# Kernel tuning notes

Hardware: AMD Instinct MI355X
Metric: run time of the kernel (lower is better)

## Reference

```python
import jax, jax.numpy as jnp
import numpy as np

N_E = 1024     # codebook size (n_e, nbooks=1)
E_DIM = 256    # embedding dim
BETA = 0.25
B, T = 16, 4096


def setup_inputs() -> dict:
    key = jax.random.key(0)
    k1, k2 = jax.random.split(key)
    z = jax.random.normal(k1, (B, T, E_DIM), dtype=jnp.float32)
    # matches torch init: uniform(-1/n_e_i, 1/n_e_i)
    codebook = jax.random.uniform(k2, (N_E, E_DIM), dtype=jnp.float32,
                                  minval=-1.0 / N_E, maxval=1.0 / N_E)
    return {"z": z, "codebook": codebook}


def reference(z, codebook):
    zf = z.reshape(-1, E_DIM)                                   # [N, d]
    dist = (jnp.sum(zf * zf, axis=1, keepdims=True)
            - 2.0 * (zf @ codebook.T)
            + jnp.sum(codebook * codebook, axis=1)[None, :])
    idx = jnp.argmin(dist, axis=1)                              # [N]
    # one-hot scatter + matmul == codebook gather
    z_q = codebook[idx].reshape(z.shape)                        # [B, T, d]
    loss = (jnp.mean((z_q - jax.lax.stop_gradient(z)) ** 2)
            + BETA * jnp.mean((z - jax.lax.stop_gradient(z_q)) ** 2))
    # straight-through estimator
    z_q_st = z + jax.lax.stop_gradient(z_q - z)
    indices = idx.reshape(z.shape[:-1] + (1,))                  # [B, T, 1]
    return z_q_st, loss, indices
```

## Files before the change

kernel.cpp:

```cpp
#include <hip/hip_runtime.h>
#include <hip/hip_bf16.h>
#include <math.h>

typedef __bf16 bf16x8 __attribute__((ext_vector_type(8)));
typedef float f32x4 __attribute__((ext_vector_type(4)));
typedef unsigned short u16x8 __attribute__((ext_vector_type(8)));

constexpr int EDIM = 256;
constexpr int NE = 1024;
constexpr int NROWS = 65536;
constexpr float BETA = 0.25f;

constexpr size_t A2T_OFF   = 0;
constexpr size_t A2T_SZ    = (size_t)1024 * 16 * 4096;
constexpr size_t B2T_OFF   = A2T_OFF + A2T_SZ;
constexpr size_t B2T_SZ    = (size_t)8 * 16 * 8192;
constexpr size_t SZROW_OFF = B2T_OFF + B2T_SZ;
constexpr size_t SZABS_OFF = SZROW_OFF + 262144;
constexpr size_t CNORM_OFF = SZABS_OFF + 262144;
constexpr size_t BMAX_OFF  = CNORM_OFF + 4096;
constexpr size_t EMAX_OFF  = BMAX_OFF + 4096;
constexpr size_t CNT_OFF   = EMAX_OFF + 256;
constexpr size_t LIST_OFF  = CNT_OFF + 256;
constexpr size_t LPART_OFF = LIST_OFF + 262144;
constexpr size_t LP2_OFF   = LPART_OFF + 262144;
constexpr size_t WS_NEED   = LP2_OFF + 1024;

__device__ __forceinline__ unsigned short f32_to_bf16_rne(float f) {
    unsigned u = __float_as_uint(f);
    u += 0x7fffu + ((u >> 16) & 1u);
    return (unsigned short)(u >> 16);
}
__device__ __forceinline__ float bf16_to_f32(unsigned short h) {
    return __uint_as_float((unsigned)h << 16);
}

#define GLL16(g, l)                                                                   \
    __builtin_amdgcn_global_load_lds(                                                 \
        (const __attribute__((address_space(1))) unsigned int*)(g),                   \
        (__attribute__((address_space(3))) unsigned int*)(l), 16, 0, 0)

__global__ __launch_bounds__(64)
void p3_codebook(const float* __restrict__ cb, float* __restrict__ cnorm,
                 char* __restrict__ B2t, float* __restrict__ bmax) {
    __shared__ float xr[256];
    __shared__ float rres[16];
    __shared__ unsigned short ehi[256], elo[256];
    const int e = blockIdx.x, l = threadIdx.x;
    const float4 v = reinterpret_cast<const float4*>(cb + (size_t)e * EDIM)[l];
    *reinterpret_cast<float4*>(&xr[l * 4]) = v;
    float amax = fmaxf(fmaxf(fabsf(v.x), fabsf(v.y)), fmaxf(fabsf(v.z), fabsf(v.w)));
    #pragma unroll
    for (int off = 32; off; off >>= 1) amax = fmaxf(amax, __shfl_down(amax, off));
    __syncthreads();
    #pragma unroll
    for (int i = 0; i < 4; ++i) {
        const int idx = i * 64 + l;
        const float f = xr[idx];
        const unsigned short h = f32_to_bf16_rne(f);
        ehi[idx] = h;
        elo[idx] = f32_to_bf16_rne(f - bf16_to_f32(h));
    }
    if (l < 16) {
        const float* x = xr + (l >> 3) * 128;
        const int j = l & 7;
        float r = __fmul_rn(x[j], x[j]);
        for (int i = 8; i < 128; i += 8) r = __fadd_rn(r, __fmul_rn(x[i + j], x[i + j]));
        rres[l] = r;
    }
    __syncthreads();
    if (l == 0) {
        float h0 = __fadd_rn(__fadd_rn(__fadd_rn(rres[0], rres[1]), __fadd_rn(rres[2], rres[3])),
                             __fadd_rn(__fadd_rn(rres[4], rres[5]), __fadd_rn(rres[6], rres[7])));
        float h1 = __fadd_rn(__fadd_rn(__fadd_rn(rres[8], rres[9]), __fadd_rn(rres[10], rres[11])),
                             __fadd_rn(__fadd_rn(rres[12], rres[13]), __fadd_rn(rres[14], rres[15])));
        cnorm[e] = __fadd_rn(h0, h1);
        bmax[e] = amax;
    }
    {
        const int c = l >> 2, kgv = l & 3;
        const int colbase = ((c < 8) ? c * 32 : (c - 8) * 32) + kgv * 8;
        const unsigned short* src = (c < 8) ? ehi : elo;
        char* dst = B2t + ((((size_t)(e >> 7) * 16 + c) * 512 + (size_t)kgv * 128 + (e & 127)) * 16);
        *reinterpret_cast<uint4*>(dst) = *reinterpret_cast<const uint4*>(&src[colbase]);
    }
}

__global__ void k_emax(const float* __restrict__ bmax, float* __restrict__ emax, int* cnt) {
    __shared__ float red[256];
    if (threadIdx.x == 0) cnt[0] = 0;
    float m = 0.f;
    for (int i = threadIdx.x; i < NE; i += 256) m = fmaxf(m, bmax[i]);
    red[threadIdx.x] = m;
    __syncthreads();
    for (int h = 128; h; h >>= 1) {
        if (threadIdx.x < h) red[threadIdx.x] = fmaxf(red[threadIdx.x], red[threadIdx.x + h]);
        __syncthreads();
    }
    if (threadIdx.x == 0) emax[0] = red[0];
}

__global__ __launch_bounds__(256)
void p2_atile(const float* __restrict__ z, char* __restrict__ A2t,
              float* __restrict__ szrow, float* __restrict__ szabs) {
    __shared__ float t[64][260];
    __shared__ float ch[64][16];
    const int mt = blockIdx.x, h = blockIdx.y, tid = threadIdx.x;
    const int mt64 = mt * 2 + h;
    const int row0 = mt64 * 64;
    #pragma unroll
    for (int i = 0; i < 16; ++i) {
        const int fid = i * 256 + tid;
        const int r = fid >> 6, c4 = fid & 63;
        const float4 v = *reinterpret_cast<const float4*>(
            z + (size_t)(row0 + r) * EDIM + c4 * 4);
        *reinterpret_cast<float4*>(&t[r][c4 * 4]) = v;
    }
    __syncthreads();
    {
        const int r = tid >> 2, q = tid & 3;
        float asum = 0.f;
        for (int c = 0; c < 64; ++c) asum += fabsf(t[r][q * 64 + c]);
        asum += __shfl_xor(asum, 1);
        asum += __shfl_xor(asum, 2);
        #pragma unroll
        for (int cc = 0; cc < 4; ++cc) {
            const int chain = q * 4 + cc;
            const float* x = &t[r][(chain >> 3) * 128];
            const int j = chain & 7;
            float rr = __fmul_rn(x[j], x[j]);
            for (int i = 8; i < 128; i += 8) rr = __fadd_rn(rr, __fmul_rn(x[i + j], x[i + j]));
            ch[r][chain] = rr;
        }
        __syncthreads();
        if (q == 0) {
            const float* c0 = ch[r];
            const float h0 = __fadd_rn(__fadd_rn(__fadd_rn(c0[0], c0[1]), __fadd_rn(c0[2], c0[3])),
                                       __fadd_rn(__fadd_rn(c0[4], c0[5]), __fadd_rn(c0[6], c0[7])));
            const float h1 = __fadd_rn(__fadd_rn(__fadd_rn(c0[8], c0[9]), __fadd_rn(c0[10], c0[11])),
                                       __fadd_rn(__fadd_rn(c0[12], c0[13]), __fadd_rn(c0[14], c0[15])));
            szrow[row0 + r] = __fadd_rn(h0, h1);
            szabs[row0 + r] = asum;
        }
    }
    #pragma unroll
    for (int i = 0; i < 16; ++i) {
        const int sid = i * 256 + tid;
        const int ca = sid >> 8, kgv = (sid >> 6) & 3, rwl = sid & 63;
        const int cbase = ((ca < 8) ? ca : ca - 8) * 32 + kgv * 8;
        u16x8 out;
        #pragma unroll
        for (int j = 0; j < 8; ++j) {
            const float f = t[rwl][cbase + j];
            unsigned short h16 = f32_to_bf16_rne(f);
            if (ca >= 8) h16 = f32_to_bf16_rne(f - bf16_to_f32(h16));
            out[j] = h16;
        }
        char* dst = A2t + ((((size_t)mt64 * 16 + ca) * 256 + (size_t)kgv * 64 + rwl) * 16);
        *reinterpret_cast<u16x8*>(dst) = out;
    }
}

__global__ __launch_bounds__(256, 2)
void vq_main(const char* __restrict__ A2t, const char* __restrict__ B2t,
             const float* __restrict__ cnorm, const float* __restrict__ szrow,
             const float* __restrict__ szabs, const float* __restrict__ emaxp,
             const float* __restrict__ cb,
             float* __restrict__ idxf, int* __restrict__ cnt, int* __restrict__ list,
             float* __restrict__ zq, float* __restrict__ lpart) {
    constexpr int CNS = 65536;
    __shared__ char smem[69632] __attribute__((aligned(16)));
    float* cns = reinterpret_cast<float*>(smem + CNS);
    float (*ms1)[2] = reinterpret_cast<float(*)[2]>(smem);
    float (*ms2)[2] = reinterpret_cast<float(*)[2]>(smem + 512);
    int   (*mi1)[2] = reinterpret_cast<int(*)[2]>(smem + 1024);
    int*  bidx      = reinterpret_cast<int*>(smem + 1536);

    const int tid = threadIdx.x;
    const int mtile = blockIdx.x;
    const size_t rowbase = (size_t)mtile * 64;
    const int l = tid & 63, wid = tid >> 6;
    const int kg = l >> 4, li = l & 15;
    const int wr = wid >> 1, wc = wid & 1;

    GLL16((const char*)cnorm + tid * 16, smem + CNS + tid * 16);
    const char* Ag = A2t + (size_t)mtile * 65536;
    #pragma unroll
    for (int i = 0; i < 16; ++i)
        GLL16(Ag + (i * 256 + tid) * 16, smem + (i * 256 + tid) * 16);
    asm volatile("s_waitcnt vmcnt(0)" ::: "memory");
    __syncthreads();

    int aoff[2], boff[4];
    #pragma unroll
    for (int f = 0; f < 2; ++f)
        aoff[f] = kg * 1024 + (wr * 32 + f * 16 + li) * 16;
    #pragma unroll
    for (int f = 0; f < 4; ++f)
        boff[f] = kg * 2048 + (wc * 64 + f * 16 + li) * 16;

    bf16x8 cAh[2], cAl[2], cB[4];
    #pragma unroll
    for (int f = 0; f < 2; ++f) {
        cAh[f] = *reinterpret_cast<const bf16x8*>(smem + 0 * 4096 + aoff[f]);
        cAl[f] = *reinterpret_cast<const bf16x8*>(smem + 8 * 4096 + aoff[f]);
    }
    #pragma unroll
    for (int f = 0; f < 4; ++f)
        cB[f] = *reinterpret_cast<const bf16x8*>(B2t + boff[f]);

    float s1v[2][4], s2v[2][4];
    int i1v[2][4];
    #pragma unroll
    for (int a = 0; a < 2; ++a)
        #pragma unroll
        for (int b = 0; b < 4; ++b) { s1v[a][b] = 3.4e38f; s2v[a][b] = 3.4e38f; i1v[a][b] = 0; }

    for (int nt = 0; nt < 8; ++nt) {
        f32x4 acc[2][4];
        const f32x4 zf4 = {0.f, 0.f, 0.f, 0.f};
        #pragma unroll
        for (int a = 0; a < 2; ++a)
            #pragma unroll
            for (int b = 0; b < 4; ++b) acc[a][b] = zf4;

        #pragma unroll
        for (int j = 0; j < 16; ++j) {
            const int g = nt * 16 + j;
            bf16x8 nAh[2], nAl[2], nB[4];
            {
                const int jn = (j + 1) & 15;
                const char* gB = B2t + (size_t)(g + 1) * 8192;
                #pragma unroll
                for (int f = 0; f < 4; ++f)
                    nB[f] = *reinterpret_cast<const bf16x8*>(gB + boff[f]);
                if (jn < 8) {
                    #pragma unroll
                    for (int f = 0; f < 2; ++f) {
                        nAh[f] = *reinterpret_cast<const bf16x8*>(smem + jn * 4096 + aoff[f]);
                        nAl[f] = *reinterpret_cast<const bf16x8*>(smem + (8 + jn) * 4096 + aoff[f]);
                    }
                } else {
                    #pragma unroll
                    for (int f = 0; f < 2; ++f) {
                        nAh[f] = *reinterpret_cast<const bf16x8*>(smem + (jn - 8) * 4096 + aoff[f]);
                        nAl[f] = cAl[f];
                    }
                }
            }
            #pragma unroll
            for (int fm = 0; fm < 2; ++fm)
                #pragma unroll
                for (int fn = 0; fn < 4; ++fn)
                    acc[fm][fn] = __builtin_amdgcn_mfma_f32_16x16x32_bf16(cAh[fm], cB[fn], acc[fm][fn], 0, 0, 0);
            if (j < 8) {
                #pragma unroll
                for (int fm = 0; fm < 2; ++fm)
                    #pragma unroll
                    for (int fn = 0; fn < 4; ++fn)
                        acc[fm][fn] = __builtin_amdgcn_mfma_f32_16x16x32_bf16(cAl[fm], cB[fn], acc[fm][fn], 0, 0, 0);
            }
            #pragma unroll
            for (int f = 0; f < 2; ++f) { cAh[f] = nAh[f]; cAl[f] = nAl[f]; }
            #pragma unroll
            for (int f = 0; f < 4; ++f) cB[f] = nB[f];
        }

        const int ntb = nt * 128;
        #pragma unroll
        for (int fn = 0; fn < 4; ++fn) {
            const int e = ntb + wc * 64 + fn * 16 + li;
            const float cn = cns[e];
            #pragma unroll
            for (int fm = 0; fm < 2; ++fm)
                #pragma unroll
                for (int r = 0; r < 4; ++r) {
                    const float s = cn - 2.0f * acc[fm][fn][r];
                    if (s < s1v[fm][r]) { s2v[fm][r] = s1v[fm][r]; s1v[fm][r] = s; i1v[fm][r] = e; }
                    else s2v[fm][r] = fminf(s2v[fm][r], s);
                }
        }
    }

    __syncthreads();

    #pragma unroll
    for (int fm = 0; fm < 2; ++fm)
        #pragma unroll
        for (int r = 0; r < 4; ++r) {
            float s1 = s1v[fm][r], s2 = s2v[fm][r];
            int i1 = i1v[fm][r];
            #pragma unroll
            for (int off = 1; off < 16; off <<= 1) {
                const float os1 = __shfl_xor(s1, off);
                const float os2 = __shfl_xor(s2, off);
                const int oi1 = __shfl_xor(i1, off);
                const bool take = (os1 < s1) || (os1 == s1 && oi1 < i1);
                const float loser = take ? s1 : os1;
                if (take) { s1 = os1; i1 = oi1; }
                s2 = fminf(fminf(s2, os2), loser);
            }
            if (li == 0) {
                const int rloc = wr * 32 + fm * 16 + (kg << 2) + r;
                ms1[rloc][wc] = s1; ms2[rloc][wc] = s2; mi1[rloc][wc] = i1;
            }
        }
    __syncthreads();

    if (tid < 64) {
        const float a1 = ms1[tid][0], b1 = ms1[tid][1];
        const float a2 = ms2[tid][0], b2 = ms2[tid][1];
        const int ai = mi1[tid][0], bi = mi1[tid][1];
        const bool take = (b1 < a1) || (b1 == a1 && bi < ai);
        const float s1 = take ? b1 : a1;
        const int i1 = take ? bi : ai;
        const float loser = take ? a1 : b1;
        const float s2 = fminf(fminf(a2, b2), loser);
        const int rowg = (int)rowbase + tid;
        const float szv = szrow[rowg], sab = szabs[rowg];
        const float M = 2.0e-4f * sab * emaxp[0] + ldexpf(1.0f, ilogbf(szv * 1.02f) - 23);
        idxf[rowg] = (float)i1;
        lpart[rowg] = s1 + szv;
        bidx[tid] = i1;
        if (s2 - s1 <= 2.0f * M) { const int p = atomicAdd(cnt, 1); list[p] = rowg; }
    }
    __syncthreads();

    {
        const float4* cb4 = reinterpret_cast<const float4*>(cb);
        float4* zq4 = reinterpret_cast<float4*>(zq);
        #pragma unroll 4
        for (int j = 0; j < 16; ++j) {
            const int rr = wid * 16 + j;
            const int e = bidx[rr];
            zq4[(rowbase + rr) * 64 + l] = cb4[(size_t)e * 64 + l];
        }
    }
}

__global__ __launch_bounds__(256)
void vq_rescan(const float* __restrict__ z, const float* __restrict__ cb,
               const float* __restrict__ cnorm, const float* __restrict__ szrow,
               const int* __restrict__ list, const int* __restrict__ cntp,
               float* __restrict__ idxf, float* __restrict__ zq, float* __restrict__ lpart) {
    __shared__ float zr[8][260];
    __shared__ float szs[8];
    __shared__ int rows_s[8];
    __shared__ float sred[256];
    __shared__ int ired[256];
    const int tid = threadIdx.x;
    const int n = cntp[0];
    const int groups = (n + 7) >> 3;
    for (int g = blockIdx.x; g < groups; g += gridDim.x) {
        if (tid < 8) {
            const int gi = g * 8 + tid;
            const int row = (gi < n) ? list[gi] : -1;
            rows_s[tid] = row;
            szs[tid] = (row >= 0) ? szrow[row] : 0.f;
        }
        __syncthreads();
        #pragma unroll
        for (int i = 0; i < 8; ++i) {
            const int sid = i * 256 + tid;
            const int rr = sid >> 8, k = sid & 255;
            if (rows_s[rr] >= 0) zr[rr][k] = z[(size_t)rows_s[rr] * EDIM + k];
        }
        __syncthreads();
        float bs[8];
        int bi[8];
        #pragma unroll
        for (int rr = 0; rr < 8; ++rr) { bs[rr] = 3.4e38f; bi[rr] = 0; }
        for (int q = 0; q < 4; ++q) {
            const int e = tid + q * 256;
            const float4* crow = reinterpret_cast<const float4*>(cb + (size_t)e * EDIM);
            float d[8];
            #pragma unroll
            for (int rr = 0; rr < 8; ++rr) d[rr] = 0.f;
            for (int k4 = 0; k4 < 64; ++k4) {
                const float4 c4 = crow[k4];
                #pragma unroll
                for (int rr = 0; rr < 8; ++rr) {
                    d[rr] = fmaf(zr[rr][k4 * 4 + 0], c4.x, d[rr]);
                    d[rr] = fmaf(zr[rr][k4 * 4 + 1], c4.y, d[rr]);
                    d[rr] = fmaf(zr[rr][k4 * 4 + 2], c4.z, d[rr]);
                    d[rr] = fmaf(zr[rr][k4 * 4 + 3], c4.w, d[rr]);
                }
            }
            const float cn = cnorm[e];
            #pragma unroll
            for (int rr = 0; rr < 8; ++rr) {
                const float b1 = __fadd_rn(szs[rr], __fmul_rn(-2.0f, d[rr]));
                const float s = __fadd_rn(b1, cn);
                if (s < bs[rr]) { bs[rr] = s; bi[rr] = e; }
            }
        }
        #pragma unroll
        for (int rr = 0; rr < 8; ++rr) {
            sred[tid] = bs[rr];
            ired[tid] = bi[rr];
            __syncthreads();
            for (int h = 128; h; h >>= 1) {
                if (tid < h) {
                    const float so = sred[tid + h];
                    const int io = ired[tid + h];
                    if (so < sred[tid] || (so == sred[tid] && io < ired[tid])) {
                        sred[tid] = so; ired[tid] = io;
                    }
                }
                __syncthreads();
            }
            if (rows_s[rr] >= 0) {
                const int best = ired[0];
                const int row = rows_s[rr];
                zq[(size_t)row * EDIM + tid] = cb[(size_t)best * EDIM + tid];
                if (tid == 0) { idxf[row] = (float)best; lpart[row] = sred[0]; }
            }
            __syncthreads();
        }
    }
}

__global__ void vq_loss1(const float* __restrict__ lpart, float* __restrict__ lp2) {
    __shared__ float red[256];
    const int t = threadIdx.x;
    red[t] = lpart[blockIdx.x * 256 + t];
    __syncthreads();
    for (int h = 128; h; h >>= 1) {
        if (t < h) red[t] += red[t + h];
        __syncthreads();
    }
    if (t == 0) lp2[blockIdx.x] = red[0];
}
__global__ void vq_loss2(const float* __restrict__ lp2, float* __restrict__ outloss) {
    __shared__ float red[256];
    const int t = threadIdx.x;
    red[t] = lp2[t];
    __syncthreads();
    for (int h = 128; h; h >>= 1) {
        if (t < h) red[t] += red[t + h];
        __syncthreads();
    }
    if (t == 0) outloss[0] = red[0] * ((1.0f + BETA) / 16777216.0f);
}

__device__ __forceinline__ float np_sum128_sq(const float* __restrict__ x) {
    float r[8];
    #pragma unroll
    for (int j = 0; j < 8; ++j) r[j] = __fmul_rn(x[j], x[j]);
    #pragma unroll
    for (int i = 8; i < 128; i += 8)
        #pragma unroll
        for (int j = 0; j < 8; ++j) r[j] = __fadd_rn(r[j], __fmul_rn(x[i + j], x[i + j]));
    return __fadd_rn(__fadd_rn(__fadd_rn(r[0], r[1]), __fadd_rn(r[2], r[3])),
                     __fadd_rn(__fadd_rn(r[4], r[5]), __fadd_rn(r[6], r[7])));
}
__global__ void fb_prep(const float* __restrict__ z, const float* __restrict__ cb,
                        float* __restrict__ szrow, float* __restrict__ cnorm) {
    int t = blockIdx.x * blockDim.x + threadIdx.x;
    if (t < NROWS) {
        const float* x = z + (size_t)t * EDIM;
        szrow[t] = __fadd_rn(np_sum128_sq(x), np_sum128_sq(x + 128));
    } else if (t < NROWS + NE) {
        const float* x = cb + (size_t)(t - NROWS) * EDIM;
        cnorm[t - NROWS] = __fadd_rn(np_sum128_sq(x), np_sum128_sq(x + 128));
    }
}
__global__ __launch_bounds__(256, 2)
void fb_vq(const float* __restrict__ z, const float* __restrict__ cb,
           const float* __restrict__ cnorm, const float* __restrict__ szrow,
           float* __restrict__ zq, float* __restrict__ idxf, float* __restrict__ lpart) {
    __shared__ float As[64 * 268];
    __shared__ float Bs[32 * 68];
    __shared__ int bidx[64];
    __shared__ float lred[4];
    const int tid = threadIdx.x;
    const int tx = tid & 15, ty = tid >> 4;
    const size_t rowbase = (size_t)blockIdx.x * 64;
    const float4* zg = reinterpret_cast<const float4*>(z + rowbase * EDIM);
    #pragma unroll
    for (int it = 0; it < 16; ++it) {
        int id = it * 256 + tid;
        int r = id >> 6, c4 = id & 63;
        float4 v = zg[id];
        *reinterpret_cast<float4*>(&As[r * 268 + c4 * 4]) = v;
    }
    float sz[4];
    #pragma unroll
    for (int m = 0; m < 4; ++m) sz[m] = szrow[rowbase + ty * 4 + m];
    float bestS[4]; int bestI[4];
    #pragma unroll
    for (int m = 0; m < 4; ++m) { bestS[m] = 3.4e38f; bestI[m] = 0; }
    for (int nt = 0; nt < NE / 64; ++nt) {
        float acc[4][4];
        #pragma unroll
        for (int m = 0; m < 4; ++m)
            #pragma unroll
            for (int n = 0; n < 4; ++n) acc[m][n] = 0.f;
        const int ebase = nt * 64;
        for (int k0 = 0; k0 < EDIM; k0 += 32) {
            __syncthreads();
            #pragma unroll
            for (int i = 0; i < 8; ++i) {
                int id = i * 256 + tid;
                int n = id >> 5, k = id & 31;
                Bs[k * 68 + n] = cb[(size_t)(ebase + n) * EDIM + k0 + k];
            }
            __syncthreads();
            #pragma unroll
            for (int kg2 = 0; kg2 < 32; kg2 += 4) {
                float4 a[4], b[4];
                #pragma unroll
                for (int m = 0; m < 4; ++m)
                    a[m] = *reinterpret_cast<const float4*>(&As[(ty * 4 + m) * 268 + k0 + kg2]);
                #pragma unroll
                for (int kk = 0; kk < 4; ++kk)
                    b[kk] = *reinterpret_cast<const float4*>(&Bs[(kg2 + kk) * 68 + tx * 4]);
                #pragma unroll
                for (int m = 0; m < 4; ++m) {
                    const float* av = reinterpret_cast<const float*>(&a[m]);
                    #pragma unroll
                    for (int kk = 0; kk < 4; ++kk) {
                        acc[m][0] = fmaf(av[kk], b[kk].x, acc[m][0]);
                        acc[m][1] = fmaf(av[kk], b[kk].y, acc[m][1]);
                        acc[m][2] = fmaf(av[kk], b[kk].z, acc[m][2]);
                        acc[m][3] = fmaf(av[kk], b[kk].w, acc[m][3]);
                    }
                }
            }
        }
        #pragma unroll
        for (int n = 0; n < 4; ++n) {
            int e = ebase + tx * 4 + n;
            float cn = cnorm[e];
            #pragma unroll
            for (int m = 0; m < 4; ++m) {
                float b1 = __fadd_rn(sz[m], __fmul_rn(-2.0f, acc[m][n]));
                float s = __fadd_rn(b1, cn);
                if (s < bestS[m]) { bestS[m] = s; bestI[m] = e; }
            }
        }
    }
    #pragma unroll
    for (int m = 0; m < 4; ++m) {
        float s = bestS[m]; int i = bestI[m];
        #pragma unroll
        for (int off = 1; off < 16; off <<= 1) {
            float s2 = __shfl_xor(s, off);
            int i2 = __shfl_xor(i, off);
            if (s2 < s || (s2 == s && i2 < i)) { s = s2; i = i2; }
        }
        if (tx == 0) bidx[ty * 4 + m] = i;
    }
    __syncthreads();
    if (tid < 64) idxf[rowbase + tid] = (float)bidx[tid];
    float lsum = 0.f;
    for (int r = 0; r < 64; ++r) {
        int e = bidx[r];
        float c = cb[(size_t)e * EDIM + tid];
        float zv = As[r * 268 + tid];
        float d = c - zv;
        lsum = fmaf(d, d, lsum);
        zq[(rowbase + r) * EDIM + tid] = c;
    }
    #pragma unroll
    for (int off = 32; off; off >>= 1) lsum += __shfl_down(lsum, off);
    if ((tid & 63) == 0) lred[tid >> 6] = lsum;
    __syncthreads();
    if (tid == 0) lpart[blockIdx.x] = lred[0] + lred[1] + lred[2] + lred[3];
}
__global__ void fb_loss(const float* __restrict__ lpart, float* __restrict__ out_loss) {
    __shared__ float red[256];
    int tid = threadIdx.x;
    float s = 0.f;
    for (int i = tid; i < NROWS / 64; i += 256) s += lpart[i];
    red[tid] = s;
    __syncthreads();
    for (int h = 128; h; h >>= 1) {
        if (tid < h) red[tid] += red[tid + h];
        __syncthreads();
    }
    if (tid == 0) out_loss[0] = red[0] * (1.0f + BETA) / (float)((size_t)NROWS * EDIM);
}

extern "C" void kernel_launch(void* const* d_in, const int* in_sizes, int n_in,
                              void* d_out, int out_size, void* d_ws, size_t ws_size,
                              hipStream_t stream) {
    const float* z = (const float*)d_in[0];
    const float* cb = (const float*)d_in[1];
    float* out = (float*)d_out;
    float* zq = out;
    float* loss = out + (size_t)NROWS * EDIM;
    float* idxf = loss + 1;
    char* ws = (char*)d_ws;

    if (ws_size < WS_NEED) {
        float* cnorm = (float*)ws;
        float* szrow = cnorm + NE;
        float* lpart = szrow + NROWS;
        hipLaunchKernelGGL(fb_prep, dim3((NROWS + NE + 255) / 256), dim3(256), 0, stream, z, cb, szrow, cnorm);
        hipLaunchKernelGGL(fb_vq, dim3(NROWS / 64), dim3(256), 0, stream, z, cb, cnorm, szrow, zq, idxf, lpart);
        hipLaunchKernelGGL(fb_loss, dim3(1), dim3(256), 0, stream, lpart, loss);
        return;
    }

    char* A2t = ws + A2T_OFF;
    char* B2t = ws + B2T_OFF;
    float* szrow = (float*)(ws + SZROW_OFF);
    float* szabs = (float*)(ws + SZABS_OFF);
    float* cnorm = (float*)(ws + CNORM_OFF);
    float* bmax = (float*)(ws + BMAX_OFF);
    float* emax = (float*)(ws + EMAX_OFF);
    int* cnt = (int*)(ws + CNT_OFF);
    int* list = (int*)(ws + LIST_OFF);
    float* lpart = (float*)(ws + LPART_OFF);
    float* lp2 = (float*)(ws + LP2_OFF);

    hipLaunchKernelGGL(p3_codebook, dim3(NE), dim3(64), 0, stream, cb, cnorm, B2t, bmax);
    hipLaunchKernelGGL(k_emax, dim3(1), dim3(256), 0, stream, bmax, emax, cnt);
    hipLaunchKernelGGL(p2_atile, dim3(512, 2), dim3(256), 0, stream, z, A2t, szrow, szabs);
    hipLaunchKernelGGL(vq_main, dim3(1024), dim3(256), 0, stream,
                       A2t, B2t, cnorm, szrow, szabs, emax, cb, idxf, cnt, list, zq, lpart);
    hipLaunchKernelGGL(vq_rescan, dim3(1024), dim3(256), 0, stream,
                       z, cb, cnorm, szrow, list, cnt, idxf, zq, lpart);
    hipLaunchKernelGGL(vq_loss1, dim3(256), dim3(256), 0, stream, lpart, lp2);
    hipLaunchKernelGGL(vq_loss2, dim3(1), dim3(256), 0, stream, lp2, loss);
}
```

Before: 244.1 us.

## Fuse z tile bf16 split into main kernel and replace emax reduction with atomicMax

```diff
diff --git a/kernel.cpp b/kernel.cpp
--- a/kernel.cpp
+++ b/kernel.cpp
@@ -11,15 +11,12 @@
 constexpr int NROWS = 65536;
 constexpr float BETA = 0.25f;
 
-constexpr size_t A2T_OFF   = 0;
-constexpr size_t A2T_SZ    = (size_t)1024 * 16 * 4096;
-constexpr size_t B2T_OFF   = A2T_OFF + A2T_SZ;
+constexpr size_t B2T_OFF   = 0;
 constexpr size_t B2T_SZ    = (size_t)8 * 16 * 8192;
 constexpr size_t SZROW_OFF = B2T_OFF + B2T_SZ;
 constexpr size_t SZABS_OFF = SZROW_OFF + 262144;
 constexpr size_t CNORM_OFF = SZABS_OFF + 262144;
-constexpr size_t BMAX_OFF  = CNORM_OFF + 4096;
-constexpr size_t EMAX_OFF  = BMAX_OFF + 4096;
+constexpr size_t EMAX_OFF  = CNORM_OFF + 4096;
 constexpr size_t CNT_OFF   = EMAX_OFF + 256;
 constexpr size_t LIST_OFF  = CNT_OFF + 256;
 constexpr size_t LPART_OFF = LIST_OFF + 262144;
@@ -42,7 +39,7 @@
 
 __global__ __launch_bounds__(64)
 void p3_codebook(const float* __restrict__ cb, float* __restrict__ cnorm,
-                 char* __restrict__ B2t, float* __restrict__ bmax) {
+                 char* __restrict__ B2t, unsigned* __restrict__ emax_u) {
     __shared__ float xr[256];
     __shared__ float rres[16];
     __shared__ unsigned short ehi[256], elo[256];
@@ -75,7 +72,7 @@
         float h1 = __fadd_rn(__fadd_rn(__fadd_rn(rres[8], rres[9]), __fadd_rn(rres[10], rres[11])),
                              __fadd_rn(__fadd_rn(rres[12], rres[13]), __fadd_rn(rres[14], rres[15])));
         cnorm[e] = __fadd_rn(h0, h1);
-        bmax[e] = amax;
+        atomicMax(emax_u, __float_as_uint(amax));
     }
     {
         const int c = l >> 2, kgv = l & 3;
@@ -86,47 +83,54 @@
     }
 }
 
-__global__ void k_emax(const float* __restrict__ bmax, float* __restrict__ emax, int* cnt) {
-    __shared__ float red[256];
-    if (threadIdx.x == 0) cnt[0] = 0;
-    float m = 0.f;
-    for (int i = threadIdx.x; i < NE; i += 256) m = fmaxf(m, bmax[i]);
-    red[threadIdx.x] = m;
-    __syncthreads();
-    for (int h = 128; h; h >>= 1) {
-        if (threadIdx.x < h) red[threadIdx.x] = fmaxf(red[threadIdx.x], red[threadIdx.x + h]);
-        __syncthreads();
-    }
-    if (threadIdx.x == 0) emax[0] = red[0];
-}
-
-__global__ __launch_bounds__(256)
-void p2_atile(const float* __restrict__ z, char* __restrict__ A2t,
-              float* __restrict__ szrow, float* __restrict__ szabs) {
-    __shared__ float t[64][260];
-    __shared__ float ch[64][16];
-    const int mt = blockIdx.x, h = blockIdx.y, tid = threadIdx.x;
-    const int mt64 = mt * 2 + h;
-    const int row0 = mt64 * 64;
-    #pragma unroll
-    for (int i = 0; i < 16; ++i) {
-        const int fid = i * 256 + tid;
-        const int r = fid >> 6, c4 = fid & 63;
-        const float4 v = *reinterpret_cast<const float4*>(
-            z + (size_t)(row0 + r) * EDIM + c4 * 4);
-        *reinterpret_cast<float4*>(&t[r][c4 * 4]) = v;
-    }
-    __syncthreads();
+__global__ __launch_bounds__(256, 2)
+void vq_main(const float* __restrict__ z, const char* __restrict__ B2t,
+             const float* __restrict__ cnorm, const float* __restrict__ emaxp,
+             const float* __restrict__ cb,
+             float* __restrict__ idxf, int* __restrict__ cnt, int* __restrict__ list,
+             float* __restrict__ zq, float* __restrict__ lpart,
+             float* __restrict__ szrow, float* __restrict__ szabs) {
+    constexpr int CNS = 65536;
+    __shared__ char smem[71680] __attribute__((aligned(16)));
+    float* cns  = reinterpret_cast<float*>(smem + CNS);
+    float* szsr = reinterpret_cast<float*>(smem + 70656);
+    float* szsa = reinterpret_cast<float*>(smem + 70912);
+    float (*ms1)[2] = reinterpret_cast<float(*)[2]>(smem);
+    float (*ms2)[2] = reinterpret_cast<float(*)[2]>(smem + 512);
+    int   (*mi1)[2] = reinterpret_cast<int(*)[2]>(smem + 1024);
+    int*  bidx      = reinterpret_cast<int*>(smem + 1536);
+
+    const int tid = threadIdx.x;
+    const int mtile = blockIdx.x;
+    const size_t rowbase = (size_t)mtile * 64;
+    const int l = tid & 63, wid = tid >> 6;
+    const int kg = l >> 4, li = l & 15;
+    const int wr = wid >> 1, wc = wid & 1;
+
     {
+        float* t = reinterpret_cast<float*>(smem);
+        #pragma unroll
+        for (int i = 0; i < 16; ++i) {
+            const int fid = i * 256 + tid;
+            const int r = fid >> 6, c4 = fid & 63;
+            const float4 v = *reinterpret_cast<const float4*>(
+                z + (rowbase + r) * EDIM + c4 * 4);
+            *reinterpret_cast<float4*>(&t[r * 260 + c4 * 4]) = v;
+        }
+    }
+    __syncthreads();
+    {
+        float* t = reinterpret_cast<float*>(smem);
+        float (*ch)[16] = reinterpret_cast<float(*)[16]>(smem + 66560);
         const int r = tid >> 2, q = tid & 3;
         float asum = 0.f;
-        for (int c = 0; c < 64; ++c) asum += fabsf(t[r][q * 64 + c]);
+        for (int c = 0; c < 64; ++c) asum += fabsf(t[r * 260 + q * 64 + c]);
         asum += __shfl_xor(asum, 1);
         asum += __shfl_xor(asum, 2);
         #pragma unroll
         for (int cc = 0; cc < 4; ++cc) {
             const int chain = q * 4 + cc;
-            const float* x = &t[r][(chain >> 3) * 128];
+            const float* x = &t[r * 260 + (chain >> 3) * 128];
             const int j = chain & 7;
             float rr = __fmul_rn(x[j], x[j]);
             for (int i = 8; i < 128; i += 8) rr = __fadd_rn(rr, __fmul_rn(x[i + j], x[i + j]));
@@ -139,55 +143,40 @@
                                        __fadd_rn(__fadd_rn(c0[4], c0[5]), __fadd_rn(c0[6], c0[7])));
             const float h1 = __fadd_rn(__fadd_rn(__fadd_rn(c0[8], c0[9]), __fadd_rn(c0[10], c0[11])),
                                        __fadd_rn(__fadd_rn(c0[12], c0[13]), __fadd_rn(c0[14], c0[15])));
-            szrow[row0 + r] = __fadd_rn(h0, h1);
-            szabs[row0 + r] = asum;
-        }
-    }
-    #pragma unroll
-    for (int i = 0; i < 16; ++i) {
-        const int sid = i * 256 + tid;
-        const int ca = sid >> 8, kgv = (sid >> 6) & 3, rwl = sid & 63;
-        const int cbase = ((ca < 8) ? ca : ca - 8) * 32 + kgv * 8;
-        u16x8 out;
-        #pragma unroll
-        for (int j = 0; j < 8; ++j) {
-            const float f = t[rwl][cbase + j];
-            unsigned short h16 = f32_to_bf16_rne(f);
-            if (ca >= 8) h16 = f32_to_bf16_rne(f - bf16_to_f32(h16));
-            out[j] = h16;
-        }
-        char* dst = A2t + ((((size_t)mt64 * 16 + ca) * 256 + (size_t)kgv * 64 + rwl) * 16);
-        *reinterpret_cast<u16x8*>(dst) = out;
-    }
-}
-
-__global__ __launch_bounds__(256, 2)
-void vq_main(const char* __restrict__ A2t, const char* __restrict__ B2t,
-             const float* __restrict__ cnorm, const float* __restrict__ szrow,
-             const float* __restrict__ szabs, const float* __restrict__ emaxp,
-             const float* __restrict__ cb,
-             float* __restrict__ idxf, int* __restrict__ cnt, int* __restrict__ list,
-             float* __restrict__ zq, float* __restrict__ lpart) {
-    constexpr int CNS = 65536;
-    __shared__ char smem[69632] __attribute__((aligned(16)));
-    float* cns = reinterpret_cast<float*>(smem + CNS);
-    float (*ms1)[2] = reinterpret_cast<float(*)[2]>(smem);
-    float (*ms2)[2] = reinterpret_cast<float(*)[2]>(smem + 512);
-    int   (*mi1)[2] = reinterpret_cast<int(*)[2]>(smem + 1024);
-    int*  bidx      = reinterpret_cast<int*>(smem + 1536);
-
-    const int tid = threadIdx.x;
-    const int mtile = blockIdx.x;
-    const size_t rowbase = (size_t)mtile * 64;
-    const int l = tid & 63, wid = tid >> 6;
-    const int kg = l >> 4, li = l & 15;
-    const int wr = wid >> 1, wc = wid & 1;
-
+            const float sz = __fadd_rn(h0, h1);
+            szsr[r] = sz; szsa[r] = asum;
+            szrow[rowbase + r] = sz;
+            szabs[rowbase + r] = asum;
+        }
+    }
+    u16x8 chi[8], clo[8];
+    {
+        float* t = reinterpret_cast<float*>(smem);
+        const int r = tid >> 2, q = tid & 3;
+        #pragma unroll
+        for (int s = 0; s < 8; ++s) {
+            u16x8 h, lw;
+            #pragma unroll
+            for (int j = 0; j < 8; ++j) {
+                const float f = t[r * 260 + q * 64 + s * 8 + j];
+                const unsigned short hh = f32_to_bf16_rne(f);
+                h[j] = hh;
+                lw[j] = f32_to_bf16_rne(f - bf16_to_f32(hh));
+            }
+            chi[s] = h; clo[s] = lw;
+        }
+    }
+    __syncthreads();
+    {
+        const int r = tid >> 2, q = tid & 3;
+        #pragma unroll
+        for (int s = 0; s < 8; ++s) {
+            const int ca = 2 * q + (s >> 2), kgv = s & 3;
+            *reinterpret_cast<u16x8*>(smem + (ca * 256 + kgv * 64 + r) * 16) = chi[s];
+            *reinterpret_cast<u16x8*>(smem + ((8 + ca) * 256 + kgv * 64 + r) * 16) = clo[s];
+        }
+    }
     GLL16((const char*)cnorm + tid * 16, smem + CNS + tid * 16);
-    const char* Ag = A2t + (size_t)mtile * 65536;
-    #pragma unroll
-    for (int i = 0; i < 16; ++i)
-        GLL16(Ag + (i * 256 + tid) * 16, smem + (i * 256 + tid) * 16);
     asm volatile("s_waitcnt vmcnt(0)" ::: "memory");
     __syncthreads();
 
@@ -317,7 +306,7 @@
         const float loser = take ? a1 : b1;
         const float s2 = fminf(fminf(a2, b2), loser);
         const int rowg = (int)rowbase + tid;
-        const float szv = szrow[rowg], sab = szabs[rowg];
+        const float szv = szsr[tid], sab = szsa[tid];
         const float M = 2.0e-4f * sab * emaxp[0] + ldexpf(1.0f, ilogbf(szv * 1.02f) - 23);
         idxf[rowg] = (float)i1;
         lpart[rowg] = s1 + szv;
@@ -603,23 +592,21 @@
         return;
     }
 
-    char* A2t = ws + A2T_OFF;
     char* B2t = ws + B2T_OFF;
     float* szrow = (float*)(ws + SZROW_OFF);
     float* szabs = (float*)(ws + SZABS_OFF);
     float* cnorm = (float*)(ws + CNORM_OFF);
-    float* bmax = (float*)(ws + BMAX_OFF);
     float* emax = (float*)(ws + EMAX_OFF);
     int* cnt = (int*)(ws + CNT_OFF);
     int* list = (int*)(ws + LIST_OFF);
     float* lpart = (float*)(ws + LPART_OFF);
     float* lp2 = (float*)(ws + LP2_OFF);
 
-    hipLaunchKernelGGL(p3_codebook, dim3(NE), dim3(64), 0, stream, cb, cnorm, B2t, bmax);
-    hipLaunchKernelGGL(k_emax, dim3(1), dim3(256), 0, stream, bmax, emax, cnt);
-    hipLaunchKernelGGL(p2_atile, dim3(512, 2), dim3(256), 0, stream, z, A2t, szrow, szabs);
+    hipMemsetAsync(emax, 0, 4, stream);
+    hipMemsetAsync(cnt, 0, 4, stream);
+    hipLaunchKernelGGL(p3_codebook, dim3(NE), dim3(64), 0, stream, cb, cnorm, B2t, (unsigned*)emax);
     hipLaunchKernelGGL(vq_main, dim3(1024), dim3(256), 0, stream,
-                       A2t, B2t, cnorm, szrow, szabs, emax, cb, idxf, cnt, list, zq, lpart);
+                       z, B2t, cnorm, emax, cb, idxf, cnt, list, zq, lpart, szrow, szabs);
     hipLaunchKernelGGL(vq_rescan, dim3(1024), dim3(256), 0, stream,
                        z, cb, cnorm, szrow, list, cnt, idxf, zq, lpart);
     hipLaunchKernelGGL(vq_loss1, dim3(256), dim3(256), 0, stream, lpart, lp2);
```

Result: faster. 237.5 us (median of 2 runs) (-2.7%).
